# Performance work log

Measured on AMD Instinct MI355X. Metric: run time of the kernel, lower is better.

Reference implementation:

```python
import jax, jax.numpy as jnp
import numpy as np
from math import sqrt

B, N, D = 8, 4096, 512

def rotary(x, phases):
    # x: [B,N,D], phases: [B,N,D/2]
    c, s = jnp.cos(phases), jnp.sin(phases)
    a, b = jnp.split(x, 2, axis=-1)
    return jnp.concatenate([a * c - b * s, a * s + b * c], axis=-1)

def setup_inputs() -> dict:
    key = jax.random.key(0)
    ks = jax.random.split(key, 8)
    phi = jax.random.normal(ks[0], (B, N, D), dtype=jnp.float32)
    coords = jax.random.normal(ks[1], (B, N, 3), dtype=jnp.float32)
    weights = jax.random.uniform(ks[2], (B, N), dtype=jnp.float32)
    std = 1.0 / sqrt(D)
    Wq = jax.random.normal(ks[3], (D, D), dtype=jnp.float32) * std
    Wk = jax.random.normal(ks[4], (D, D), dtype=jnp.float32) * std
    Wv = jax.random.normal(ks[5], (D, D), dtype=jnp.float32) * std
    bq = jnp.zeros((D,), jnp.float32)
    bk = jnp.zeros((D,), jnp.float32)
    bv = jnp.zeros((D,), jnp.float32)
    # mode_lift weight, std = 1/kernel_scale with kernel_scale=1.0
    Wrot = jax.random.normal(ks[6], (D // 2, 3), dtype=jnp.float32)
    return {"phi": phi, "coords": coords, "weights": weights,
            "Wq": Wq, "bq": bq, "Wk": Wk, "bk": bk, "Wv": Wv, "bv": bv,
            "Wrot": Wrot}

def reference(phi, coords, weights, Wq, bq, Wk, bk, Wv, bv, Wrot):
    d = phi.shape[-1]
    q = phi @ Wq.T + bq
    k = phi @ Wk.T + bk
    v = phi @ Wv.T + bv
    # _normalize: scale query by 1/sqrt(d); attach quadrature weights to value
    q = q * (1.0 / sqrt(d))
    v = weights[..., None] * v
    # rotary positional encoding on q and k
    phases = jnp.einsum('bnc,dc->bnd', coords, Wrot)  # [B,N,D/2]
    q = rotary(q, phases)
    k = rotary(k, phases)
    # linear attention: q @ (k^T @ v), O(N*d^2)
    kv = jnp.einsum('bnd,bne->bde', k, v)   # [B,D,D]
    return jnp.einsum('bnd,bde->bne', q, kv)  # [B,N,D]
```

## Files before the change

### kernel.cpp

```cpp
#include <hip/hip_runtime.h>


typedef _Float16 f16x8 __attribute__((ext_vector_type(8)));
typedef _Float16 f16x4 __attribute__((ext_vector_type(4)));
typedef float f32x4 __attribute__((ext_vector_type(4)));

__device__ __forceinline__ void gl_lds16(const void* g, void* l) {
    __builtin_amdgcn_global_load_lds(
        (const __attribute__((address_space(1))) void*)g,
        (__attribute__((address_space(3))) void*)l, 16, 0, 0);
}

__device__ __forceinline__ void stage2(const _Float16* gA, size_t sA,
                                       const _Float16* gB, size_t sB,
                                       _Float16* As, _Float16* Bs,
                                       int ca, int srow, int sseg) {
    gl_lds16(&gA[(size_t)(ca * 16 + srow) * sA + sseg], &As[ca * 512]);
    gl_lds16(&gA[(size_t)(ca * 16 + 16 + srow) * sA + sseg], &As[(ca + 1) * 512]);
    gl_lds16(&gB[(size_t)(ca * 16 + srow) * sB + sseg], &Bs[ca * 512]);
    gl_lds16(&gB[(size_t)(ca * 16 + 16 + srow) * sB + sseg], &Bs[(ca + 1) * 512]);
}

__device__ __forceinline__ void mfma_step(const _Float16* As, const _Float16* Bs,
                                          int wm, int wn, int l16, int qs,
                                          f32x4 acc[4][4]) {
    f16x8 af[4], bf[4];
    #pragma unroll
    for (int mi = 0; mi < 4; mi++)
        af[mi] = *(const f16x8*)&As[(wm + mi * 16 + l16) * 32 + qs * 8];
    #pragma unroll
    for (int ni = 0; ni < 4; ni++)
        bf[ni] = *(const f16x8*)&Bs[(wn + ni * 16 + l16) * 32 + qs * 8];
    #pragma unroll
    for (int mi = 0; mi < 4; mi++)
        #pragma unroll
        for (int ni = 0; ni < 4; ni++)
            acc[mi][ni] = __builtin_amdgcn_mfma_f32_16x16x32_f16(
                af[mi], bf[ni], acc[mi][ni], 0, 0, 0);
}

#define PHASE(BUFA, BUFB, VM)                                                 \
    asm volatile("s_waitcnt vmcnt(" #VM ")" ::: "memory");                    \
    __builtin_amdgcn_s_barrier();                                             \
    asm volatile("" ::: "memory");                                            \
    __builtin_amdgcn_sched_barrier(0);                                        \
    __builtin_amdgcn_s_setprio(1);                                            \
    mfma_step(BUFA, BUFB, wm, wn, l16, qs, acc);                              \
    __builtin_amdgcn_s_setprio(0);                                            \
    asm volatile("s_waitcnt lgkmcnt(0)" ::: "memory");                        \
    __builtin_amdgcn_sched_barrier(0);                                        \
    __builtin_amdgcn_s_barrier();                                             \
    asm volatile("" ::: "memory");

#define PIPE_LOOP(gA, sA, gB, sB)                                             \
    stage2(gA, sA, gB, sB, As0, Bs0, ca, srow, sseg);                         \
    stage2(gA + 32, sA, gB + 32, sB, As1, Bs1, ca, srow, sseg);               \
    _Pragma("unroll")                                                         \
    for (int p = 0; p < 8; p++) {                                             \
        const int t0 = 2 * p;                                                 \
        PHASE(As0, Bs0, 4)                                                    \
        if (t0 + 2 < 16)                                                      \
            stage2(gA + (size_t)(t0 + 2) * 32, sA,                            \
                   gB + (size_t)(t0 + 2) * 32, sB,                            \
                   As0, Bs0, ca, srow, sseg);                                 \
        if (p < 7) { PHASE(As1, Bs1, 4) }                                     \
        else       { PHASE(As1, Bs1, 0) }                                     \
        if (t0 + 3 < 16)                                                      \
            stage2(gA + (size_t)(t0 + 3) * 32, sA,                            \
                   gB + (size_t)(t0 + 3) * 32, sB,                            \
                   As1, Bs1, ca, srow, sseg);                                 \
    }

__global__ __launch_bounds__(256) void convert_phi(const float* __restrict__ phi,
                                                   _Float16* __restrict__ phi_h) {
    int i = (blockIdx.x * 256 + threadIdx.x) * 4;
    float4 v = *(const float4*)(phi + i);
    f16x4 o = {(_Float16)v.x, (_Float16)v.y, (_Float16)v.z, (_Float16)v.w};
    *(f16x4*)(phi_h + i) = o;
}

__global__ __launch_bounds__(256) void pack_w(
    const float* __restrict__ Wq, const float* __restrict__ Wk,
    const float* __restrict__ Wv, const float* __restrict__ bq,
    const float* __restrict__ bk, const float* __restrict__ bv,
    _Float16* __restrict__ wcat, float* __restrict__ bcat) {
    int j = blockIdx.x;
    int reg = j >> 9, jr = j & 511;
    const float* W; const float* bias;
    if (reg == 0)      { W = Wq; bias = bq; }
    else if (reg == 1) { W = Wk; bias = bk; }
    else               { W = Wv; bias = bv; }
    int d = (reg < 2) ? ((jr & 1) ? (jr >> 1) + 256 : (jr >> 1)) : jr;
    for (int i = threadIdx.x; i < 512; i += 256)
        wcat[j * 512 + i] = (_Float16)W[d * 512 + i];
    if (threadIdx.x == 0) bcat[j] = bias[d];
}

__global__ __launch_bounds__(256) void qkv_kernel(
    const _Float16* __restrict__ phi_h, const _Float16* __restrict__ wcat,
    const float* __restrict__ bcat, const float* __restrict__ coords,
    const float* __restrict__ weights, const float* __restrict__ Wrot,
    _Float16* __restrict__ qr, _Float16* __restrict__ krT,
    _Float16* __restrict__ vwT) {
    __shared__ __align__(16) char smem[34816];
    _Float16* As0 = (_Float16*)smem;
    _Float16* Bs0 = (_Float16*)(smem + 8192);
    _Float16* As1 = (_Float16*)(smem + 16384);
    _Float16* Bs1 = (_Float16*)(smem + 24576);
    _Float16* Ts  = (_Float16*)smem;

    const int tid = threadIdx.x;
    const int lane = tid & 63, wave = tid >> 6;
    const int quad = lane >> 4, l16 = lane & 15;
    const int qs = quad ^ ((l16 >> 1) & 3);
    const int wm = (wave >> 1) * 64, wn = (wave & 1) * 64;
    const int flat = blockIdx.x + blockIdx.y * 12;
    const int swz = (flat & 7) * 384 + (flat >> 3);
    const int c0 = (swz % 12) * 128;
    const int m0 = (swz / 12) * 128;
    const int ca = wave * 2;
    const int srow = lane >> 2;
    const int sseg = (((lane & 3) ^ ((lane >> 3) & 3)) * 8);

    const _Float16* gA = phi_h + (size_t)m0 * 512;
    const _Float16* gB = wcat + (size_t)c0 * 512;

    f32x4 acc[4][4] = {};

    PIPE_LOOP(gA, 512, gB, 512)

    const int region = c0 >> 9;
    const float qscale = 0.04419417382415922f;

    float bias[4], w0[4], w1[4], w2[4];
    #pragma unroll
    for (int ni = 0; ni < 4; ni++) {
        int gc = c0 + wn + ni * 16 + l16;
        bias[ni] = bcat[gc];
        if (region < 2) {
            int jp = (gc & 511) >> 1;
            w0[ni] = Wrot[jp * 3];
            w1[ni] = Wrot[jp * 3 + 1];
            w2[ni] = Wrot[jp * 3 + 2];
        }
    }

    if (region == 0) {
        #pragma unroll
        for (int mi = 0; mi < 4; mi++)
            #pragma unroll
            for (int r = 0; r < 4; r++) {
                int row = wm + mi * 16 + quad * 4 + r;
                int gm = m0 + row;
                float x = coords[gm * 3], y = coords[gm * 3 + 1], z = coords[gm * 3 + 2];
                #pragma unroll
                for (int ni = 0; ni < 4; ni++) {
                    float val = (acc[mi][ni][r] + bias[ni]) * qscale;
                    float part = __shfl_xor(val, 1);
                    float ph = x * w0[ni] + y * w1[ni] + z * w2[ni];
                    float sv, cv; __sincosf(ph, &sv, &cv);
                    float res = (l16 & 1) ? (part * sv + val * cv)
                                          : (val * cv - part * sv);
                    Ts[row * 136 + wn + ni * 16 + l16] = (_Float16)res;
                }
            }
        __syncthreads();
        for (int i = tid; i < 2048; i += 256) {
            int row = i >> 4, cv = (i & 15) * 8;
            *(f16x8*)&qr[(m0 + row) * 512 + c0 + cv] = *(f16x8*)&Ts[row * 136 + cv];
        }
    } else {
        #pragma unroll
        for (int mi = 0; mi < 4; mi++)
            #pragma unroll
            for (int r = 0; r < 4; r++) {
                int row = wm + mi * 16 + quad * 4 + r;
                int gm = m0 + row;
                if (region == 1) {
                    float x = coords[gm * 3], y = coords[gm * 3 + 1], z = coords[gm * 3 + 2];
                    #pragma unroll
                    for (int ni = 0; ni < 4; ni++) {
                        float val = acc[mi][ni][r] + bias[ni];
                        float part = __shfl_xor(val, 1);
                        float ph = x * w0[ni] + y * w1[ni] + z * w2[ni];
                        float sv, cv; __sincosf(ph, &sv, &cv);
                        float res = (l16 & 1) ? (part * sv + val * cv)
                                              : (val * cv - part * sv);
                        Ts[(wn + ni * 16 + l16) * 136 + row] = (_Float16)res;
                    }
                } else {
                    float wgt = weights[gm];
                    #pragma unroll
                    for (int ni = 0; ni < 4; ni++) {
                        float val = (acc[mi][ni][r] + bias[ni]) * wgt;
                        Ts[(wn + ni * 16 + l16) * 136 + row] = (_Float16)val;
                    }
                }
            }
        __syncthreads();
        _Float16* dst = (region == 1) ? krT : vwT;
        const int b = m0 >> 12, n0 = m0 & 4095, cb = c0 & 511;
        for (int i = tid; i < 2048; i += 256) {
            int col = i >> 4, rv = (i & 15) * 8;
            *(f16x8*)&dst[((size_t)b * 512 + cb + col) * 4096 + n0 + rv] =
                *(f16x8*)&Ts[col * 136 + rv];
        }
    }
}

__global__ __launch_bounds__(256) void kv_kernel(
    const _Float16* __restrict__ vwT, const _Float16* __restrict__ krT,
    _Float16* __restrict__ kvp) {
    __shared__ __align__(16) char smem[32768];
    _Float16* As0 = (_Float16*)smem;
    _Float16* Bs0 = (_Float16*)(smem + 8192);
    _Float16* As1 = (_Float16*)(smem + 16384);
    _Float16* Bs1 = (_Float16*)(smem + 24576);
    const int tid = threadIdx.x, lane = tid & 63, wave = tid >> 6;
    const int quad = lane >> 4, l16 = lane & 15;
    const int qs = quad ^ ((l16 >> 1) & 3);
    const int wm = (wave >> 1) * 64, wn = (wave & 1) * 64;
    const int flat = blockIdx.x + blockIdx.y * 4 + blockIdx.z * 16;
    const int swz = (flat & 7) * 128 + (flat >> 3);
    const int d0 = (swz & 3) * 128, e0 = ((swz >> 2) & 3) * 128;
    const int zz = swz >> 4;
    const int b = zz >> 3, split = zz & 7;
    const int ca = wave * 2;
    const int srow = lane >> 2;
    const int sseg = (((lane & 3) ^ ((lane >> 3) & 3)) * 8);
    const size_t base = (size_t)b * 512 * 4096;
    const int kbeg = split * 512;
    const _Float16* gA = vwT + base + (size_t)e0 * 4096 + kbeg;
    const _Float16* gB = krT + base + (size_t)d0 * 4096 + kbeg;
    f32x4 acc[4][4] = {};

    PIPE_LOOP(gA, 4096, gB, 4096)

    _Float16* dst = kvp + ((size_t)split * 8 + b) * 262144;
    #pragma unroll
    for (int mi = 0; mi < 4; mi++)
        #pragma unroll
        for (int ni = 0; ni < 4; ni++)
            #pragma unroll
            for (int r = 0; r < 4; r++) {
                int e = e0 + wm + mi * 16 + quad * 4 + r;
                int d = d0 + wn + ni * 16 + l16;
                dst[e * 512 + d] = (_Float16)acc[mi][ni][r];
            }
}

__global__ __launch_bounds__(256) void reduce_kv(const _Float16* __restrict__ kvp,
                                                 _Float16* __restrict__ kvT) {
    int i = (blockIdx.x * 256 + threadIdx.x) * 8;
    float s[8] = {};
    #pragma unroll
    for (int sp = 0; sp < 8; sp++) {
        f16x8 v = *(const f16x8*)(kvp + (size_t)sp * 2097152 + i);
        #pragma unroll
        for (int j = 0; j < 8; j++) s[j] += (float)v[j];
    }
    f16x8 o;
    #pragma unroll
    for (int j = 0; j < 8; j++) o[j] = (_Float16)s[j];
    *(f16x8*)(kvT + i) = o;
}

__global__ __launch_bounds__(256) void out_kernel(
    const _Float16* __restrict__ qr, const _Float16* __restrict__ kvT,
    float* __restrict__ out) {
    __shared__ __align__(16) char smem[32768];
    _Float16* As0 = (_Float16*)smem;
    _Float16* Bs0 = (_Float16*)(smem + 8192);
    _Float16* As1 = (_Float16*)(smem + 16384);
    _Float16* Bs1 = (_Float16*)(smem + 24576);
    const int tid = threadIdx.x, lane = tid & 63, wave = tid >> 6;
    const int quad = lane >> 4, l16 = lane & 15;
    const int qs = quad ^ ((l16 >> 1) & 3);
    const int wm = (wave >> 1) * 64, wn = (wave & 1) * 64;
    const int flat = blockIdx.x + blockIdx.y * 4;
    const int swz = (flat & 7) * 128 + (flat >> 3);
    const int e0 = (swz & 3) * 128, m0 = (swz >> 2) * 128;
    const int b = m0 >> 12;
    const int ca = wave * 2;
    const int srow = lane >> 2;
    const int sseg = (((lane & 3) ^ ((lane >> 3) & 3)) * 8);
    const _Float16* gA = qr + (size_t)m0 * 512;
    const _Float16* gB = kvT + (size_t)b * 262144 + (size_t)e0 * 512;
    f32x4 acc[4][4] = {};

    PIPE_LOOP(gA, 512, gB, 512)

    #pragma unroll
    for (int mi = 0; mi < 4; mi++)
        #pragma unroll
        for (int ni = 0; ni < 4; ni++)
            #pragma unroll
            for (int r = 0; r < 4; r++) {
                int gm = m0 + wm + mi * 16 + quad * 4 + r;
                int e = e0 + wn + ni * 16 + l16;
                out[(size_t)gm * 512 + e] = acc[mi][ni][r];
            }
}

extern "C" void kernel_launch(void* const* d_in, const int* in_sizes, int n_in,
                              void* d_out, int out_size, void* d_ws, size_t ws_size,
                              hipStream_t stream) {
    const float* phi     = (const float*)d_in[0];
    const float* coords  = (const float*)d_in[1];
    const float* weights = (const float*)d_in[2];
    const float* Wq      = (const float*)d_in[3];
    const float* bq      = (const float*)d_in[4];
    const float* Wk      = (const float*)d_in[5];
    const float* bk      = (const float*)d_in[6];
    const float* Wv      = (const float*)d_in[7];
    const float* bv      = (const float*)d_in[8];
    const float* Wrot    = (const float*)d_in[9];
    float* out = (float*)d_out;

    char* ws = (char*)d_ws;
    _Float16* phi_h = (_Float16*)(ws);
    _Float16* kvp   = (_Float16*)(ws);
    _Float16* wcat  = (_Float16*)(ws + 33554432);
    float*    bcat  = (float*)   (ws + 35127296);
    _Float16* qr    = (_Float16*)(ws + 35133440);
    _Float16* krT   = (_Float16*)(ws + 68687872);
    _Float16* vwT   = (_Float16*)(ws + 102242304);
    _Float16* kvT   = (_Float16*)(ws + 135796736);

    convert_phi<<<16384, 256, 0, stream>>>(phi, phi_h);
    pack_w<<<1536, 256, 0, stream>>>(Wq, Wk, Wv, bq, bk, bv, wcat, bcat);
    qkv_kernel<<<dim3(12, 256), 256, 0, stream>>>(phi_h, wcat, bcat, coords,
                                                  weights, Wrot, qr, krT, vwT);
    kv_kernel<<<dim3(4, 4, 64), 256, 0, stream>>>(vwT, krT, kvp);
    reduce_kv<<<1024, 256, 0, stream>>>(kvp, kvT);
    out_kernel<<<dim3(4, 256), 256, 0, stream>>>(qr, kvT, out);
}
```

Measured before the change: 271.8 us.

## Switch GEMM mainloops to triple-buffered LDS ring with one barrier per step

Replaces the double-buffered two-barrier-per-tile pipeline in the qkv, kv and out GEMM kernels with a three-slot LDS ring. The next-next tile is issued before the current tile's MFMAs, so only one barrier per K-step is needed and loads get more time to land. LDS per block grows from 32-34KB to 48KB, which may lower occupancy. An extra __syncthreads is added before the qkv epilogue reuses shared memory.

```diff
diff --git a/kernel.cpp b/kernel.cpp
--- a/kernel.cpp
+++ b/kernel.cpp
@@ -39,37 +39,32 @@
                 af[mi], bf[ni], acc[mi][ni], 0, 0, 0);
 }
 
-#define PHASE(BUFA, BUFB, VM)                                                 \
-    asm volatile("s_waitcnt vmcnt(" #VM ")" ::: "memory");                    \
-    __builtin_amdgcn_s_barrier();                                             \
-    asm volatile("" ::: "memory");                                            \
-    __builtin_amdgcn_sched_barrier(0);                                        \
-    __builtin_amdgcn_s_setprio(1);                                            \
-    mfma_step(BUFA, BUFB, wm, wn, l16, qs, acc);                              \
-    __builtin_amdgcn_s_setprio(0);                                            \
-    asm volatile("s_waitcnt lgkmcnt(0)" ::: "memory");                        \
-    __builtin_amdgcn_sched_barrier(0);                                        \
-    __builtin_amdgcn_s_barrier();                                             \
-    asm volatile("" ::: "memory");
-
-#define PIPE_LOOP(gA, sA, gB, sB)                                             \
-    stage2(gA, sA, gB, sB, As0, Bs0, ca, srow, sseg);                         \
-    stage2(gA + 32, sA, gB + 32, sB, As1, Bs1, ca, srow, sseg);               \
+#define PIPE_LOOP3(gA, sA, gB, sB)                                            \
+    stage2(gA, sA, gB, sB, Asr[0], Bsr[0], ca, srow, sseg);                   \
+    stage2(gA + 32, sA, gB + 32, sB, Asr[1], Bsr[1], ca, srow, sseg);         \
     _Pragma("unroll")                                                         \
-    for (int p = 0; p < 8; p++) {                                             \
-        const int t0 = 2 * p;                                                 \
-        PHASE(As0, Bs0, 4)                                                    \
-        if (t0 + 2 < 16)                                                      \
-            stage2(gA + (size_t)(t0 + 2) * 32, sA,                            \
-                   gB + (size_t)(t0 + 2) * 32, sB,                            \
-                   As0, Bs0, ca, srow, sseg);                                 \
-        if (p < 7) { PHASE(As1, Bs1, 4) }                                     \
-        else       { PHASE(As1, Bs1, 0) }                                     \
-        if (t0 + 3 < 16)                                                      \
-            stage2(gA + (size_t)(t0 + 3) * 32, sA,                            \
-                   gB + (size_t)(t0 + 3) * 32, sB,                            \
-                   As1, Bs1, ca, srow, sseg);                                 \
+    for (int t = 0; t < 16; t++) {                                            \
+        asm volatile("s_waitcnt lgkmcnt(0)" ::: "memory");                    \
+        __builtin_amdgcn_sched_barrier(0);                                    \
+        if (t < 15) { asm volatile("s_waitcnt vmcnt(4)" ::: "memory"); }      \
+        else        { asm volatile("s_waitcnt vmcnt(0)" ::: "memory"); }      \
+        __builtin_amdgcn_s_barrier();                                         \
+        asm volatile("" ::: "memory");                                        \
+        __builtin_amdgcn_sched_barrier(0);                                    \
+        if (t + 2 < 16)                                                       \
+            stage2(gA + (size_t)(t + 2) * 32, sA,                             \
+                   gB + (size_t)(t + 2) * 32, sB,                             \
+                   Asr[(t + 2) % 3], Bsr[(t + 2) % 3], ca, srow, sseg);       \
+        __builtin_amdgcn_s_setprio(1);                                        \
+        mfma_step(Asr[t % 3], Bsr[t % 3], wm, wn, l16, qs, acc);              \
+        __builtin_amdgcn_s_setprio(0);                                        \
     }
+
+#define RING_PTRS(smem)                                                       \
+    _Float16* Asr[3] = {(_Float16*)(smem), (_Float16*)(smem + 16384),         \
+                        (_Float16*)(smem + 32768)};                           \
+    _Float16* Bsr[3] = {(_Float16*)(smem + 8192), (_Float16*)(smem + 24576),  \
+                        (_Float16*)(smem + 40960)};
 
 __global__ __launch_bounds__(256) void convert_phi(const float* __restrict__ phi,
                                                    _Float16* __restrict__ phi_h) {
@@ -102,12 +97,9 @@
     const float* __restrict__ weights, const float* __restrict__ Wrot,
     _Float16* __restrict__ qr, _Float16* __restrict__ krT,
     _Float16* __restrict__ vwT) {
-    __shared__ __align__(16) char smem[34816];
-    _Float16* As0 = (_Float16*)smem;
-    _Float16* Bs0 = (_Float16*)(smem + 8192);
-    _Float16* As1 = (_Float16*)(smem + 16384);
-    _Float16* Bs1 = (_Float16*)(smem + 24576);
-    _Float16* Ts  = (_Float16*)smem;
+    __shared__ __align__(16) char smem[49152];
+    RING_PTRS(smem)
+    _Float16* Ts = (_Float16*)smem;
 
     const int tid = threadIdx.x;
     const int lane = tid & 63, wave = tid >> 6;
@@ -127,7 +119,9 @@
 
     f32x4 acc[4][4] = {};
 
-    PIPE_LOOP(gA, 512, gB, 512)
+    PIPE_LOOP3(gA, 512, gB, 512)
+
+    __syncthreads();
 
     const int region = c0 >> 9;
     const float qscale = 0.04419417382415922f;
@@ -211,11 +205,8 @@
 __global__ __launch_bounds__(256) void kv_kernel(
     const _Float16* __restrict__ vwT, const _Float16* __restrict__ krT,
     _Float16* __restrict__ kvp) {
-    __shared__ __align__(16) char smem[32768];
-    _Float16* As0 = (_Float16*)smem;
-    _Float16* Bs0 = (_Float16*)(smem + 8192);
-    _Float16* As1 = (_Float16*)(smem + 16384);
-    _Float16* Bs1 = (_Float16*)(smem + 24576);
+    __shared__ __align__(16) char smem[49152];
+    RING_PTRS(smem)
     const int tid = threadIdx.x, lane = tid & 63, wave = tid >> 6;
     const int quad = lane >> 4, l16 = lane & 15;
     const int qs = quad ^ ((l16 >> 1) & 3);
@@ -234,7 +225,7 @@
     const _Float16* gB = krT + base + (size_t)d0 * 4096 + kbeg;
     f32x4 acc[4][4] = {};
 
-    PIPE_LOOP(gA, 4096, gB, 4096)
+    PIPE_LOOP3(gA, 4096, gB, 4096)
 
     _Float16* dst = kvp + ((size_t)split * 8 + b) * 262144;
     #pragma unroll
@@ -268,11 +259,8 @@
 __global__ __launch_bounds__(256) void out_kernel(
     const _Float16* __restrict__ qr, const _Float16* __restrict__ kvT,
     float* __restrict__ out) {
-    __shared__ __align__(16) char smem[32768];
-    _Float16* As0 = (_Float16*)smem;
-    _Float16* Bs0 = (_Float16*)(smem + 8192);
-    _Float16* As1 = (_Float16*)(smem + 16384);
-    _Float16* Bs1 = (_Float16*)(smem + 24576);
+    __shared__ __align__(16) char smem[49152];
+    RING_PTRS(smem)
     const int tid = threadIdx.x, lane = tid & 63, wave = tid >> 6;
     const int quad = lane >> 4, l16 = lane & 15;
     const int qs = quad ^ ((l16 >> 1) & 3);
@@ -288,7 +276,7 @@
     const _Float16* gB = kvT + (size_t)b * 262144 + (size_t)e0 * 512;
     f32x4 acc[4][4] = {};
 
-    PIPE_LOOP(gA, 512, gB, 512)
+    PIPE_LOOP3(gA, 512, gB, 512)
 
     #pragma unroll
     for (int mi = 0; mi < 4; mi++)
```

Measured after the change: 275.1 us. About the same (+1.2%).
